# Performance work log

Hardware: AMD Instinct MI355X
Metric: run time of the kernel (lower is better)

Reference implementation:

```python
import jax, jax.numpy as jnp
import numpy as np

B, DX, DY, H = 512, 128, 128, 512


def setup_inputs() -> dict:
    key = jax.random.key(0)
    ks = jax.random.split(key, 5)
    x = jax.random.normal(ks[0], (B, DX), dtype=jnp.float32)
    y = jax.random.normal(ks[1], (B, DY), dtype=jnp.float32)
    # torch nn.Linear-style weights [out_features, in_features], small init scale
    W1 = jax.random.normal(ks[2], (H, DX + DY), dtype=jnp.float32) * 0.05
    b1 = jnp.zeros((H,), dtype=jnp.float32)
    W2 = jax.random.normal(ks[3], (H, H), dtype=jnp.float32) * 0.05
    b2 = jnp.zeros((H,), dtype=jnp.float32)
    W3 = jax.random.normal(ks[4], (1, H), dtype=jnp.float32) * 0.05
    b3 = jnp.zeros((1,), dtype=jnp.float32)
    return {"x": x, "y": y, "W1": W1, "b1": b1, "W2": W2, "b2": b2, "W3": W3, "b3": b3}


def reference(x, y, W1, b1, W2, b2, W3, b3):
    # Original: pair (row i, col j) of the *returned* (transposed) matrix is
    # f(concat(x[i], y[j])). We fuse the B^2 concat + first Linear into two
    # B x H matmuls broadcast-summed (mathematically identical).
    dimX = x.shape[1]
    hx = jnp.einsum("id,hd->ih", x, W1[:, :dimX])          # [B, H]
    hy = jnp.einsum("jd,hd->jh", y, W1[:, dimX:])          # [B, H]
    h = jax.nn.relu(hx[:, None, :] + hy[None, :, :] + b1)   # [B, B, H]
    h = jax.nn.relu(jnp.einsum("ijh,kh->ijk", h, W2) + b2)  # [B, B, H]
    out = jnp.einsum("ijh,h->ij", h, W3[0]) + b3[0]         # [B, B]
    return out
```

## Files before the change

### kernel.cpp

```cpp
#include <hip/hip_runtime.h>
#include <hip/hip_bf16.h>

#define Bn  512
#define DXn 128
#define Hn  512

using bf16x8 = __attribute__((ext_vector_type(8))) short;
using f32x4  = __attribute__((ext_vector_type(4))) float;

static __device__ __forceinline__ unsigned int pkbf(float lo, float hi) {
    union { __hip_bfloat162 b; unsigned int u; } cv;
    cv.b = __float22bfloat162_rn(make_float2(lo, hi));
    return cv.u;
}

__global__ __launch_bounds__(256) void prep_fused(
    const float* __restrict__ x, const float* __restrict__ y,
    const float* __restrict__ W1, const float* __restrict__ b1,
    const float* __restrict__ W2,
    float* __restrict__ hxb, float* __restrict__ hyv,
    unsigned short* __restrict__ w2s)
{
    const int bid = blockIdx.x;
    const int t = threadIdx.x;

    if (bid >= 256) {
        const int T = (bid - 256) * 256 + t;
        const int l  = T & 63;
        const int hf = (T >> 6) & 15;
        const int kf = T >> 10;
        const int row = kf * 16 + (l & 15);
        const int col = hf * 32 + (l >> 4) * 8;
        const float* p = &W2[row * Hn + col];
        const float4 v0 = *(const float4*)p;
        const float4 v1 = *(const float4*)(p + 4);
        uint4 pk;
        pk.x = pkbf(v0.x, v0.y);
        pk.y = pkbf(v0.z, v0.w);
        pk.z = pkbf(v1.x, v1.y);
        pk.w = pkbf(v1.z, v1.w);
        *(uint4*)(w2s + (size_t)T * 8) = pk;
        return;
    }

    const int which = bid >> 7;
    const int rem = bid & 127;
    const int i0 = (rem >> 3) * 32;
    const int h0 = (rem & 7) * 64;
    const float* __restrict__ src = which ? y : x;
    float* __restrict__ dst = which ? hyv : hxb;
    const int off = which ? DXn : 0;

    __shared__ float xs[32][132];
    __shared__ float ws[64][132];
    #pragma unroll
    for (int it = 0; it < 4; ++it) {
        const int fi = it * 256 + t;
        const int r = fi >> 5, q = fi & 31;
        *(float4*)&xs[r][q * 4] = *(const float4*)&src[(i0 + r) * DXn + q * 4];
    }
    #pragma unroll
    for (int it = 0; it < 8; ++it) {
        const int fi = it * 256 + t;
        const int r = fi >> 5, q = fi & 31;
        *(float4*)&ws[r][q * 4] = *(const float4*)&W1[(h0 + r) * (2 * DXn) + off + q * 4];
    }
    __syncthreads();

    const int tx = t & 15;
    const int ty = t >> 4;
    float acc[2][4];
    #pragma unroll
    for (int v = 0; v < 2; ++v)
        #pragma unroll
        for (int u = 0; u < 4; ++u)
            acc[v][u] = which ? 0.0f : b1[h0 + tx + u * 16];

    #pragma unroll 4
    for (int c4 = 0; c4 < 32; ++c4) {
        const float4 xv0 = *(const float4*)&xs[ty * 2 + 0][c4 * 4];
        const float4 xv1 = *(const float4*)&xs[ty * 2 + 1][c4 * 4];
        #pragma unroll
        for (int u = 0; u < 4; ++u) {
            const float4 wv = *(const float4*)&ws[tx + u * 16][c4 * 4];
            acc[0][u] = fmaf(xv0.x, wv.x, fmaf(xv0.y, wv.y, fmaf(xv0.z, wv.z, fmaf(xv0.w, wv.w, acc[0][u]))));
            acc[1][u] = fmaf(xv1.x, wv.x, fmaf(xv1.y, wv.y, fmaf(xv1.z, wv.z, fmaf(xv1.w, wv.w, acc[1][u]))));
        }
    }
    #pragma unroll
    for (int v = 0; v < 2; ++v)
        #pragma unroll
        for (int u = 0; u < 4; ++u)
            dst[(size_t)(i0 + ty * 2 + v) * Hn + h0 + tx + u * 16] = acc[v][u];
}

__global__ __launch_bounds__(512, 2) void critic_main(
    const float* __restrict__ hxb, const float* __restrict__ hyv,
    const unsigned short* __restrict__ w2s, const float* __restrict__ b2,
    const float* __restrict__ W3, const float* __restrict__ b3,
    float* __restrict__ out)
{
    __shared__ __align__(16) unsigned char smem[131072];
    unsigned short* a_lds = (unsigned short*)smem;
    float* red = (float*)smem;

    const int i   = blockIdx.y;
    const int j0  = blockIdx.x * 128;
    const int tid = threadIdx.x;
    const int w   = tid >> 6;
    const int l   = tid & 63;
    const int lg  = l >> 4;
    const int lm  = l & 15;

    {
        const int r = w * 16 + lm;
        const float* __restrict__ hyrow = &hyv[(size_t)(j0 + r) * Hn];
        const float* __restrict__ hxrow = &hxb[(size_t)i * Hn];
        #pragma unroll
        for (int q = 0; q < 16; ++q) {
            const int h0 = q * 32 + lg * 8;
            const float4 a0 = *(const float4*)(hyrow + h0);
            const float4 a1 = *(const float4*)(hyrow + h0 + 4);
            const float4 x0 = *(const float4*)(hxrow + h0);
            const float4 x1 = *(const float4*)(hxrow + h0 + 4);
            uint4 pk;
            pk.x = pkbf(fmaxf(a0.x + x0.x, 0.f), fmaxf(a0.y + x0.y, 0.f));
            pk.y = pkbf(fmaxf(a0.z + x0.z, 0.f), fmaxf(a0.w + x0.w, 0.f));
            pk.z = pkbf(fmaxf(a1.x + x1.x, 0.f), fmaxf(a1.y + x1.y, 0.f));
            pk.w = pkbf(fmaxf(a1.z + x1.z, 0.f), fmaxf(a1.w + x1.w, 0.f));
            *(uint4*)(a_lds + ((size_t)(w * 16 + q) * 64 + l) * 8) = pk;
        }
    }
    __syncthreads();

    f32x4 acc[8][4] = {};
    const unsigned short* __restrict__ wbase =
        w2s + (size_t)(w * 4) * 16 * 64 * 8;

    bf16x8 b[2][4];
    #pragma unroll
    for (int fj = 0; fj < 4; ++fj)
        b[0][fj] = *(const bf16x8*)(wbase + ((size_t)(fj * 16) * 64 + l) * 8);

    #pragma unroll
    for (int s = 0; s < 16; ++s) {
        const int cur = s & 1, nxt = cur ^ 1;
        if (s < 15) {
            #pragma unroll
            for (int fj = 0; fj < 4; ++fj)
                b[nxt][fj] = *(const bf16x8*)(wbase + ((size_t)(fj * 16 + s + 1) * 64 + l) * 8);
        }
        bf16x8 a[8];
        #pragma unroll
        for (int fi = 0; fi < 8; ++fi)
            a[fi] = *(const bf16x8*)(a_lds + ((size_t)(fi * 16 + s) * 64 + l) * 8);
        #pragma unroll
        for (int fi = 0; fi < 8; ++fi)
            #pragma unroll
            for (int fj = 0; fj < 4; ++fj)
                acc[fi][fj] = __builtin_amdgcn_mfma_f32_16x16x32_bf16(
                    a[fi], b[cur][fj], acc[fi][fj], 0, 0, 0);
    }

    float b2v[4], w3v[4];
    #pragma unroll
    for (int fj = 0; fj < 4; ++fj) {
        const int k = w * 64 + fj * 16 + lm;
        b2v[fj] = b2[k];
        w3v[fj] = W3[k];
    }
    float rp[8][4];
    #pragma unroll
    for (int fi = 0; fi < 8; ++fi) {
        #pragma unroll
        for (int q = 0; q < 4; ++q) {
            float ssum = 0.f;
            #pragma unroll
            for (int fj = 0; fj < 4; ++fj) {
                float c = acc[fi][fj][q] + b2v[fj];
                c = fmaxf(c, 0.f);
                ssum = fmaf(c, w3v[fj], ssum);
            }
            rp[fi][q] = ssum;
        }
    }
    #pragma unroll
    for (int m = 1; m < 16; m <<= 1) {
        #pragma unroll
        for (int fi = 0; fi < 8; ++fi)
            #pragma unroll
            for (int q = 0; q < 4; ++q)
                rp[fi][q] += __shfl_xor(rp[fi][q], m, 64);
    }

    __syncthreads();
    if (lm == 0) {
        #pragma unroll
        for (int fi = 0; fi < 8; ++fi)
            #pragma unroll
            for (int q = 0; q < 4; ++q)
                red[w * 128 + fi * 16 + lg * 4 + q] = rp[fi][q];
    }
    __syncthreads();
    if (tid < 128) {
        float ssum = 0.f;
        #pragma unroll
        for (int ww = 0; ww < 8; ++ww) ssum += red[ww * 128 + tid];
        out[(size_t)i * Bn + j0 + tid] = ssum + b3[0];
    }
}

extern "C" void kernel_launch(void* const* d_in, const int* in_sizes, int n_in,
                              void* d_out, int out_size, void* d_ws, size_t ws_size,
                              hipStream_t stream) {
    const float* x  = (const float*)d_in[0];
    const float* y  = (const float*)d_in[1];
    const float* W1 = (const float*)d_in[2];
    const float* b1 = (const float*)d_in[3];
    const float* W2 = (const float*)d_in[4];
    const float* b2 = (const float*)d_in[5];
    const float* W3 = (const float*)d_in[6];
    const float* b3 = (const float*)d_in[7];
    float* out = (float*)d_out;

    char* ws = (char*)d_ws;
    float* hxb = (float*)ws;
    float* hyv = (float*)(ws + (size_t)Bn * Hn * 4);
    unsigned short* w2s = (unsigned short*)(ws + (size_t)2 * Bn * Hn * 4);

    prep_fused<<<dim3(384), dim3(256), 0, stream>>>(x, y, W1, b1, W2, hxb, hyv, w2s);
    critic_main<<<dim3(Bn / 128, Bn), dim3(512), 0, stream>>>(hxb, hyv, w2s, b2, W3, b3, out);
}
```

Before: 245.8 us.

## Switch main GEMM to 32x32x16 MFMA with matching W2 and A layouts

Replaces the 16x16x32 bf16 MFMA tiles with 32x32x16 tiles. This means re-laying out the pre-swizzled W2 buffer and the LDS activation tile into 32-row fragments, and rewriting the epilogue reduction for the new accumulator layout. It also double-buffers the A fragments from LDS alongside B and raises wave priority around the MFMA block. The larger MFMA shape reduces LDS and global fragment loads per FLOP, at the cost of more complex index mapping in the reduction and a larger shuffle epilogue.

```diff
diff --git a/kernel.cpp b/kernel.cpp
--- a/kernel.cpp
+++ b/kernel.cpp
@@ -6,7 +6,7 @@
 #define Hn  512
 
 using bf16x8 = __attribute__((ext_vector_type(8))) short;
-using f32x4  = __attribute__((ext_vector_type(4))) float;
+using f32x16 = __attribute__((ext_vector_type(16))) float;
 
 static __device__ __forceinline__ unsigned int pkbf(float lo, float hi) {
     union { __hip_bfloat162 b; unsigned int u; } cv;
@@ -26,11 +26,11 @@
 
     if (bid >= 256) {
         const int T = (bid - 256) * 256 + t;
-        const int l  = T & 63;
-        const int hf = (T >> 6) & 15;
-        const int kf = T >> 10;
-        const int row = kf * 16 + (l & 15);
-        const int col = hf * 32 + (l >> 4) * 8;
+        const int l   = T & 63;
+        const int s   = (T >> 6) & 31;
+        const int kf2 = T >> 11;
+        const int row = kf2 * 32 + (l & 31);
+        const int col = s * 16 + (l >> 5) * 8;
         const float* p = &W2[row * Hn + col];
         const float4 v0 = *(const float4*)p;
         const float4 v1 = *(const float4*)(p + 4);
@@ -109,16 +109,19 @@
     const int tid = threadIdx.x;
     const int w   = tid >> 6;
     const int l   = tid & 63;
-    const int lg  = l >> 4;
-    const int lm  = l & 15;
+    const int l5  = l >> 5;
+    const int lc  = l & 31;
 
     {
-        const int r = w * 16 + lm;
+        const int rf = w & 3;
+        const int sb = (w >> 2) * 16;
+        const int r  = rf * 32 + lc;
         const float* __restrict__ hyrow = &hyv[(size_t)(j0 + r) * Hn];
         const float* __restrict__ hxrow = &hxb[(size_t)i * Hn];
         #pragma unroll
         for (int q = 0; q < 16; ++q) {
-            const int h0 = q * 32 + lg * 8;
+            const int s  = sb + q;
+            const int h0 = s * 16 + l5 * 8;
             const float4 a0 = *(const float4*)(hyrow + h0);
             const float4 a1 = *(const float4*)(hyrow + h0 + 4);
             const float4 x0 = *(const float4*)(hxrow + h0);
@@ -128,55 +131,59 @@
             pk.y = pkbf(fmaxf(a0.z + x0.z, 0.f), fmaxf(a0.w + x0.w, 0.f));
             pk.z = pkbf(fmaxf(a1.x + x1.x, 0.f), fmaxf(a1.y + x1.y, 0.f));
             pk.w = pkbf(fmaxf(a1.z + x1.z, 0.f), fmaxf(a1.w + x1.w, 0.f));
-            *(uint4*)(a_lds + ((size_t)(w * 16 + q) * 64 + l) * 8) = pk;
-        }
-    }
-    __syncthreads();
-
-    f32x4 acc[8][4] = {};
+            *(uint4*)(a_lds + ((size_t)(rf * 32 + s) * 64 + l) * 8) = pk;
+        }
+    }
+    __syncthreads();
+
+    f32x16 acc[4][2] = {};
     const unsigned short* __restrict__ wbase =
-        w2s + (size_t)(w * 4) * 16 * 64 * 8;
-
-    bf16x8 b[2][4];
-    #pragma unroll
-    for (int fj = 0; fj < 4; ++fj)
-        b[0][fj] = *(const bf16x8*)(wbase + ((size_t)(fj * 16) * 64 + l) * 8);
-
-    #pragma unroll
-    for (int s = 0; s < 16; ++s) {
+        w2s + (size_t)(w * 2) * 32 * 64 * 8;
+
+    bf16x8 a[2][4], b[2][2];
+    #pragma unroll
+    for (int fi = 0; fi < 4; ++fi)
+        a[0][fi] = *(const bf16x8*)(a_lds + ((size_t)(fi * 32) * 64 + l) * 8);
+    #pragma unroll
+    for (int fj = 0; fj < 2; ++fj)
+        b[0][fj] = *(const bf16x8*)(wbase + ((size_t)(fj * 32) * 64 + l) * 8);
+
+    #pragma unroll
+    for (int s = 0; s < 32; ++s) {
         const int cur = s & 1, nxt = cur ^ 1;
-        if (s < 15) {
-            #pragma unroll
-            for (int fj = 0; fj < 4; ++fj)
-                b[nxt][fj] = *(const bf16x8*)(wbase + ((size_t)(fj * 16 + s + 1) * 64 + l) * 8);
-        }
-        bf16x8 a[8];
-        #pragma unroll
-        for (int fi = 0; fi < 8; ++fi)
-            a[fi] = *(const bf16x8*)(a_lds + ((size_t)(fi * 16 + s) * 64 + l) * 8);
-        #pragma unroll
-        for (int fi = 0; fi < 8; ++fi)
-            #pragma unroll
-            for (int fj = 0; fj < 4; ++fj)
-                acc[fi][fj] = __builtin_amdgcn_mfma_f32_16x16x32_bf16(
-                    a[fi], b[cur][fj], acc[fi][fj], 0, 0, 0);
-    }
-
-    float b2v[4], w3v[4];
-    #pragma unroll
-    for (int fj = 0; fj < 4; ++fj) {
-        const int k = w * 64 + fj * 16 + lm;
+        if (s < 31) {
+            #pragma unroll
+            for (int fj = 0; fj < 2; ++fj)
+                b[nxt][fj] = *(const bf16x8*)(wbase + ((size_t)(fj * 32 + s + 1) * 64 + l) * 8);
+            #pragma unroll
+            for (int fi = 0; fi < 4; ++fi)
+                a[nxt][fi] = *(const bf16x8*)(a_lds + ((size_t)(fi * 32 + s + 1) * 64 + l) * 8);
+        }
+        __builtin_amdgcn_s_setprio(1);
+        #pragma unroll
+        for (int fi = 0; fi < 4; ++fi)
+            #pragma unroll
+            for (int fj = 0; fj < 2; ++fj)
+                acc[fi][fj] = __builtin_amdgcn_mfma_f32_32x32x16_bf16(
+                    a[cur][fi], b[cur][fj], acc[fi][fj], 0, 0, 0);
+        __builtin_amdgcn_s_setprio(0);
+    }
+
+    float b2v[2], w3v[2];
+    #pragma unroll
+    for (int fj = 0; fj < 2; ++fj) {
+        const int k = w * 64 + fj * 32 + lc;
         b2v[fj] = b2[k];
         w3v[fj] = W3[k];
     }
-    float rp[8][4];
-    #pragma unroll
-    for (int fi = 0; fi < 8; ++fi) {
-        #pragma unroll
-        for (int q = 0; q < 4; ++q) {
+    float rp[4][16];
+    #pragma unroll
+    for (int fi = 0; fi < 4; ++fi) {
+        #pragma unroll
+        for (int q = 0; q < 16; ++q) {
             float ssum = 0.f;
             #pragma unroll
-            for (int fj = 0; fj < 4; ++fj) {
+            for (int fj = 0; fj < 2; ++fj) {
                 float c = acc[fi][fj][q] + b2v[fj];
                 c = fmaxf(c, 0.f);
                 ssum = fmaf(c, w3v[fj], ssum);
@@ -187,25 +194,28 @@
     #pragma unroll
     for (int m = 1; m < 16; m <<= 1) {
         #pragma unroll
-        for (int fi = 0; fi < 8; ++fi)
-            #pragma unroll
-            for (int q = 0; q < 4; ++q)
+        for (int fi = 0; fi < 4; ++fi)
+            #pragma unroll
+            for (int q = 0; q < 16; ++q)
                 rp[fi][q] += __shfl_xor(rp[fi][q], m, 64);
     }
 
     __syncthreads();
-    if (lm == 0) {
-        #pragma unroll
-        for (int fi = 0; fi < 8; ++fi)
-            #pragma unroll
-            for (int q = 0; q < 4; ++q)
-                red[w * 128 + fi * 16 + lg * 4 + q] = rp[fi][q];
+    if ((l & 15) == 0) {
+        const int half = (l >> 4) & 1;
+        #pragma unroll
+        for (int fi = 0; fi < 4; ++fi)
+            #pragma unroll
+            for (int q = 0; q < 16; ++q) {
+                const int row = (q & 3) + 8 * (q >> 2) + 4 * l5;
+                red[(w * 2 + half) * 128 + fi * 32 + row] = rp[fi][q];
+            }
     }
     __syncthreads();
     if (tid < 128) {
         float ssum = 0.f;
         #pragma unroll
-        for (int ww = 0; ww < 8; ++ww) ssum += red[ww * 128 + tid];
+        for (int p = 0; p < 16; ++p) ssum += red[p * 128 + tid];
         out[(size_t)i * Bn + j0 + tid] = ssum + b3[0];
     }
 }
```

After: 280.4 us. 1.14x slower.

## Stream W2 tiles into LDS asynchronously and split A-tile generation into halves

Applied to the files above, without the earlier changes.

W2 is repacked into per-k-step chunks. Each step's B fragments are now fetched with asynchronous global-to-LDS loads into a double buffer instead of register double-buffering. The A tile (relu(hx+hy) in bf16) is built in two halves, so the second half's global reads overlap with MFMA work on the first half, and the A buffer only needs 64KB. MFMA sections are wrapped in s_setprio. The trade-off is a block barrier after every k-step and reliance on correct ordering of the async LDS loads.

```diff
diff --git a/kernel.cpp b/kernel.cpp
--- a/kernel.cpp
+++ b/kernel.cpp
@@ -12,6 +12,13 @@
     union { __hip_bfloat162 b; unsigned int u; } cv;
     cv.b = __float22bfloat162_rn(make_float2(lo, hi));
     return cv.u;
+}
+
+static __device__ __forceinline__ void gld_lds16(const void* g, void* l) {
+    __builtin_amdgcn_global_load_lds(
+        (const __attribute__((address_space(1))) unsigned int*)g,
+        (__attribute__((address_space(3))) unsigned int*)l,
+        16, 0, 0);
 }
 
 __global__ __launch_bounds__(256) void prep_fused(
@@ -26,11 +33,11 @@
 
     if (bid >= 256) {
         const int T = (bid - 256) * 256 + t;
-        const int l  = T & 63;
-        const int hf = (T >> 6) & 15;
-        const int kf = T >> 10;
-        const int row = kf * 16 + (l & 15);
-        const int col = hf * 32 + (l >> 4) * 8;
+        const int l = T & 63;
+        const int c = (T >> 6) & 31;
+        const int s = T >> 11;
+        const int row = c * 16 + (l & 15);
+        const int col = s * 32 + (l >> 4) * 8;
         const float* p = &W2[row * Hn + col];
         const float4 v0 = *(const float4*)p;
         const float4 v1 = *(const float4*)(p + 4);
@@ -94,6 +101,26 @@
             dst[(size_t)(i0 + ty * 2 + v) * Hn + h0 + tx + u * 16] = acc[v][u];
 }
 
+static __device__ __forceinline__ void gen_a_half(
+    unsigned short* a_us, const float* __restrict__ hyrow,
+    const float* __restrict__ hxrow, int p, int w, int l, int lg)
+{
+    #pragma unroll
+    for (int q = 0; q < 8; ++q) {
+        const int h0 = (p * 8 + q) * 32 + lg * 8;
+        const float4 a0 = *(const float4*)(hyrow + h0);
+        const float4 a1 = *(const float4*)(hyrow + h0 + 4);
+        const float4 x0 = *(const float4*)(hxrow + h0);
+        const float4 x1 = *(const float4*)(hxrow + h0 + 4);
+        uint4 pk;
+        pk.x = pkbf(fmaxf(a0.x + x0.x, 0.f), fmaxf(a0.y + x0.y, 0.f));
+        pk.y = pkbf(fmaxf(a0.z + x0.z, 0.f), fmaxf(a0.w + x0.w, 0.f));
+        pk.z = pkbf(fmaxf(a1.x + x1.x, 0.f), fmaxf(a1.y + x1.y, 0.f));
+        pk.w = pkbf(fmaxf(a1.z + x1.z, 0.f), fmaxf(a1.w + x1.w, 0.f));
+        *(uint4*)(a_us + ((size_t)(w * 8 + q) * 64 + l) * 8) = pk;
+    }
+}
+
 __global__ __launch_bounds__(512, 2) void critic_main(
     const float* __restrict__ hxb, const float* __restrict__ hyv,
     const unsigned short* __restrict__ w2s, const float* __restrict__ b2,
@@ -101,7 +128,8 @@
     float* __restrict__ out)
 {
     __shared__ __align__(16) unsigned char smem[131072];
-    unsigned short* a_lds = (unsigned short*)smem;
+    unsigned short* a_us = (unsigned short*)smem;
+    unsigned char* b_base = smem + 65536;
     float* red = (float*)smem;
 
     const int i   = blockIdx.y;
@@ -112,54 +140,58 @@
     const int lg  = l >> 4;
     const int lm  = l & 15;
 
-    {
-        const int r = w * 16 + lm;
-        const float* __restrict__ hyrow = &hyv[(size_t)(j0 + r) * Hn];
-        const float* __restrict__ hxrow = &hxb[(size_t)i * Hn];
-        #pragma unroll
-        for (int q = 0; q < 16; ++q) {
-            const int h0 = q * 32 + lg * 8;
-            const float4 a0 = *(const float4*)(hyrow + h0);
-            const float4 a1 = *(const float4*)(hyrow + h0 + 4);
-            const float4 x0 = *(const float4*)(hxrow + h0);
-            const float4 x1 = *(const float4*)(hxrow + h0 + 4);
-            uint4 pk;
-            pk.x = pkbf(fmaxf(a0.x + x0.x, 0.f), fmaxf(a0.y + x0.y, 0.f));
-            pk.y = pkbf(fmaxf(a0.z + x0.z, 0.f), fmaxf(a0.w + x0.w, 0.f));
-            pk.z = pkbf(fmaxf(a1.x + x1.x, 0.f), fmaxf(a1.y + x1.y, 0.f));
-            pk.w = pkbf(fmaxf(a1.z + x1.z, 0.f), fmaxf(a1.w + x1.w, 0.f));
-            *(uint4*)(a_lds + ((size_t)(w * 16 + q) * 64 + l) * 8) = pk;
-        }
-    }
+    const float* __restrict__ hxrow = &hxb[(size_t)i * Hn];
+    const int r = w * 16 + lm;
+    const float* __restrict__ hyrow = &hyv[(size_t)(j0 + r) * Hn];
+    const unsigned char* __restrict__ w2b = (const unsigned char*)w2s;
+
+    #pragma unroll
+    for (int n = 0; n < 4; ++n) {
+        const int c = w * 4 + n;
+        gld_lds16(w2b + (size_t)c * 1024 + l * 16, b_base + c * 1024);
+    }
+    gen_a_half(a_us, hyrow, hxrow, 0, w, l, lg);
     __syncthreads();
 
     f32x4 acc[8][4] = {};
-    const unsigned short* __restrict__ wbase =
-        w2s + (size_t)(w * 4) * 16 * 64 * 8;
-
-    bf16x8 b[2][4];
-    #pragma unroll
-    for (int fj = 0; fj < 4; ++fj)
-        b[0][fj] = *(const bf16x8*)(wbase + ((size_t)(fj * 16) * 64 + l) * 8);
-
-    #pragma unroll
-    for (int s = 0; s < 16; ++s) {
-        const int cur = s & 1, nxt = cur ^ 1;
-        if (s < 15) {
+
+    #pragma unroll
+    for (int p = 0; p < 2; ++p) {
+        if (p == 1) {
+            gen_a_half(a_us, hyrow, hxrow, 1, w, l, lg);
+            __syncthreads();
+        }
+        #pragma unroll
+        for (int q = 0; q < 8; ++q) {
+            const int s = p * 8 + q;
+            if (s < 15) {
+                const int sn = s + 1;
+                const int nb = sn & 1;
+                #pragma unroll
+                for (int n = 0; n < 4; ++n) {
+                    const int c = w * 4 + n;
+                    gld_lds16(w2b + (size_t)sn * 32768 + c * 1024 + l * 16,
+                              b_base + nb * 32768 + c * 1024);
+                }
+            }
+            const int cb = s & 1;
+            bf16x8 a[8], b[4];
             #pragma unroll
             for (int fj = 0; fj < 4; ++fj)
-                b[nxt][fj] = *(const bf16x8*)(wbase + ((size_t)(fj * 16 + s + 1) * 64 + l) * 8);
-        }
-        bf16x8 a[8];
-        #pragma unroll
-        for (int fi = 0; fi < 8; ++fi)
-            a[fi] = *(const bf16x8*)(a_lds + ((size_t)(fi * 16 + s) * 64 + l) * 8);
-        #pragma unroll
-        for (int fi = 0; fi < 8; ++fi)
-            #pragma unroll
-            for (int fj = 0; fj < 4; ++fj)
-                acc[fi][fj] = __builtin_amdgcn_mfma_f32_16x16x32_bf16(
-                    a[fi], b[cur][fj], acc[fi][fj], 0, 0, 0);
+                b[fj] = *(const bf16x8*)(b_base + cb * 32768 + (w * 4 + fj) * 1024 + l * 16);
+            #pragma unroll
+            for (int fi = 0; fi < 8; ++fi)
+                a[fi] = *(const bf16x8*)(a_us + ((size_t)(fi * 8 + q) * 64 + l) * 8);
+            __builtin_amdgcn_s_setprio(1);
+            #pragma unroll
+            for (int fi = 0; fi < 8; ++fi)
+                #pragma unroll
+                for (int fj = 0; fj < 4; ++fj)
+                    acc[fi][fj] = __builtin_amdgcn_mfma_f32_16x16x32_bf16(
+                        a[fi], b[fj], acc[fi][fj], 0, 0, 0);
+            __builtin_amdgcn_s_setprio(0);
+            __syncthreads();
+        }
     }
 
     float b2v[4], w3v[4];
@@ -173,15 +205,15 @@
     #pragma unroll
     for (int fi = 0; fi < 8; ++fi) {
         #pragma unroll
-        for (int q = 0; q < 4; ++q) {
+        for (int qq = 0; qq < 4; ++qq) {
             float ssum = 0.f;
             #pragma unroll
             for (int fj = 0; fj < 4; ++fj) {
-                float c = acc[fi][fj][q] + b2v[fj];
+                float c = acc[fi][fj][qq] + b2v[fj];
                 c = fmaxf(c, 0.f);
                 ssum = fmaf(c, w3v[fj], ssum);
             }
-            rp[fi][q] = ssum;
+            rp[fi][qq] = ssum;
         }
     }
     #pragma unroll
@@ -189,17 +221,16 @@
         #pragma unroll
         for (int fi = 0; fi < 8; ++fi)
             #pragma unroll
-            for (int q = 0; q < 4; ++q)
-                rp[fi][q] += __shfl_xor(rp[fi][q], m, 64);
-    }
-
-    __syncthreads();
+            for (int qq = 0; qq < 4; ++qq)
+                rp[fi][qq] += __shfl_xor(rp[fi][qq], m, 64);
+    }
+
     if (lm == 0) {
         #pragma unroll
         for (int fi = 0; fi < 8; ++fi)
             #pragma unroll
-            for (int q = 0; q < 4; ++q)
-                red[w * 128 + fi * 16 + lg * 4 + q] = rp[fi][q];
+            for (int qq = 0; qq < 4; ++qq)
+                red[w * 128 + fi * 16 + lg * 4 + qq] = rp[fi][qq];
     }
     __syncthreads();
     if (tid < 128) {
```

New measurement: 263.2 us. +7.1%, slower.
